# Performance work log

Measured on AMD Instinct MI355X. Metric: run time of the kernel, lower is better.

Reference implementation:

```python
import jax, jax.numpy as jnp
import numpy as np

NEG_W = 0.5  # negative_weight

def setup_inputs() -> dict:
    key = jax.random.key(0)
    ks = jax.random.split(key, 11)
    U, V, P, F, D, NF = 16384, 50000, 65536, 20, 64, 100000
    return {
        "user_emb": jax.random.normal(ks[0], (NF, D), jnp.float32),
        "item_emb": jax.random.normal(ks[1], (NF, D), jnp.float32),
        "w_user": jax.random.normal(ks[2], (NF,), jnp.float32),
        "w_item": jax.random.normal(ks[3], (NF,), jnp.float32),
        "bias": jax.random.normal(ks[4], (1,), jnp.float32),
        "h1": jax.random.normal(ks[5], (D,), jnp.float32),
        "h2": jax.random.normal(ks[6], (D,), jnp.float32),
        "user_feat_idx": jax.random.randint(ks[7], (U, F), 0, NF, jnp.int32),
        "item_feat_idx": jax.random.randint(ks[8], (V, F), 0, NF, jnp.int32),
        "pos_user_ids": jax.random.randint(ks[9], (P,), 0, U, jnp.int32),
        "pos_item_ids": jax.random.randint(ks[10], (P,), 0, V, jnp.int32),
    }

def _entity_terms(emb, w, feat_idx, h1, extra):
    # emb: [NF,D], feat_idx: [N,F] -> batched gather + FM bi-interaction
    g = emb[feat_idx]                      # [N,F,D]
    s = g.sum(axis=1)                      # [N,D]  (p_ud / q_vd)
    bi = 0.5 * (jnp.square(s) - jnp.square(g).sum(axis=1))  # [N,D]
    scalar = bi @ h1 + w[feat_idx].sum(axis=1) + extra       # [N]
    return s, scalar

def reference(user_emb, item_emb, w_user, w_item, bias, h1, h2,
              user_feat_idx, item_feat_idx, pos_user_ids, pos_item_ids):
    U = user_feat_idx.shape[0]
    V = item_feat_idx.shape[0]
    ones_u = jnp.ones((U, 1), user_emb.dtype)
    ones_v = jnp.ones((V, 1), item_emb.dtype)

    p_ud, su = _entity_terms(user_emb, w_user, user_feat_idx, h1, bias[0])
    q_vd, sv = _entity_terms(item_emb, w_item, item_feat_idx, h1, 0.0)
    p_u = jnp.concatenate([p_ud, su[:, None], ones_u], axis=1)  # [U,D+2]
    q_v = jnp.concatenate([q_vd, ones_v, sv[:, None]], axis=1)  # [V,D+2]

    # negative (all-pairs) term via D x D Gram matrices
    A = p_ud.T @ p_ud                                           # [D,D]
    B = q_vd.T @ q_vd                                           # [D,D]
    loss_neg = NEG_W * jnp.einsum('i,j,ij,ij->', h2, h2, A, B)

    # positive-pair term
    hv = jnp.concatenate([h2, jnp.ones((2,), h2.dtype)])        # [D+2]
    y = jnp.einsum('pd,pd,d->p', p_u[pos_user_ids], q_v[pos_item_ids], hv)
    loss_pos = jnp.sum((1.0 - NEG_W) * jnp.square(y) - 2.0 * y)

    return jnp.reshape(loss_neg + loss_pos, (1,))
```

## Files before the change

### kernel.cpp

```cpp
#include <hip/hip_runtime.h>

#define FD 20
#define DD 64

#define GA 64
#define GB 128
#define GAB 16
#define GBB 32
#define POSB 2048
#define NEGB 64

typedef float float4v __attribute__((ext_vector_type(4)));
typedef unsigned short ushort4v __attribute__((ext_vector_type(4)));
typedef unsigned short ushort8v __attribute__((ext_vector_type(8)));
typedef short short8v __attribute__((ext_vector_type(8)));

__device__ __forceinline__ unsigned short f2bf(float f) {
    unsigned u = __float_as_uint(f);
    unsigned r = u + 0x7fffu + ((u >> 16) & 1u);
    return (unsigned short)(r >> 16);
}
__device__ __forceinline__ float bf2f(unsigned short h) {
    return __uint_as_float((unsigned)h << 16);
}

__global__ __launch_bounds__(256) void conv_kernel(
    const float* __restrict__ ue, const float* __restrict__ ie,
    unsigned int* __restrict__ u8, unsigned int* __restrict__ i8,
    int n4, float* __restrict__ out, int out_size)
{
    int i = blockIdx.x * blockDim.x + threadIdx.x;
    if (i < out_size) out[i] = 0.0f;
    if (i >= 2 * n4) return;
    const float4v* src; unsigned int* dst; int k;
    if (i < n4) { src = (const float4v*)ue; dst = u8; k = i; }
    else        { src = (const float4v*)ie; dst = i8; k = i - n4; }
    float4v v = src[k];
    unsigned int p = 0;
    p = __builtin_amdgcn_cvt_pk_fp8_f32(v.x, v.y, p, false);
    p = __builtin_amdgcn_cvt_pk_fp8_f32(v.z, v.w, p, true);
    dst[k] = p;
}

__global__ __launch_bounds__(256, 4) void entity_kernel(
    const unsigned char* __restrict__ user_f8,
    const unsigned char* __restrict__ item_f8,
    const float* __restrict__ w_user, const float* __restrict__ w_item,
    const float* __restrict__ bias, const float* __restrict__ h1,
    const int* __restrict__ ufeat, const int* __restrict__ ifeat,
    unsigned short* __restrict__ p_bf, float* __restrict__ su,
    unsigned short* __restrict__ q_bf, float* __restrict__ sv,
    int U, int V)
{
    int wid  = (int)((blockIdx.x * blockDim.x + threadIdx.x) >> 6);
    int lane = threadIdx.x & 63;
    if (wid >= U + V) return;

    const unsigned char* emb; const float* wv; const int* fidx; float extra;
    unsigned short* srow; float* sc;
    if (wid < U) {
        emb = user_f8; wv = w_user; fidx = ufeat + (size_t)wid * FD;
        extra = bias[0]; srow = p_bf + (size_t)wid * DD; sc = su + wid;
    } else {
        int m = wid - U;
        emb = item_f8; wv = w_item; fidx = ifeat + (size_t)m * FD;
        extra = 0.0f; srow = q_bf + (size_t)m * DD; sc = sv + m;
    }

    int myidx = 0; float myw = 0.0f;
    if (lane < FD) {
        myidx = fidx[lane];
        myw   = wv[myidx];
    }

    int grp = lane >> 4;
    int c   = lane & 15;

    int fx[5];
#pragma unroll
    for (int i = 0; i < 5; ++i)
        fx[i] = __shfl(myidx, grp + 4 * i, 64);

    unsigned int hw[5];
#pragma unroll
    for (int i = 0; i < 5; ++i)
        hw[i] = *((const unsigned int*)(emb + (size_t)fx[i] * DD) + c);

    float4v s4 = (float4v)0.0f, ss4 = (float4v)0.0f;
#pragma unroll
    for (int i = 0; i < 5; ++i) {
        float4v g;
        g.x = __builtin_amdgcn_cvt_f32_fp8(hw[i], 0);
        g.y = __builtin_amdgcn_cvt_f32_fp8(hw[i], 1);
        g.z = __builtin_amdgcn_cvt_f32_fp8(hw[i], 2);
        g.w = __builtin_amdgcn_cvt_f32_fp8(hw[i], 3);
        s4 += g; ss4 += g * g;
    }

#pragma unroll
    for (int off = 16; off <= 32; off <<= 1) {
        float4v t, u;
        t.x = __shfl_xor(s4.x,  off, 64); t.y = __shfl_xor(s4.y,  off, 64);
        t.z = __shfl_xor(s4.z,  off, 64); t.w = __shfl_xor(s4.w,  off, 64);
        u.x = __shfl_xor(ss4.x, off, 64); u.y = __shfl_xor(ss4.y, off, 64);
        u.z = __shfl_xor(ss4.z, off, 64); u.w = __shfl_xor(ss4.w, off, 64);
        s4 += t; ss4 += u;
    }

    float part = myw;
    if (grp == 0) {
        float4v h14 = *(const float4v*)(h1 + c * 4);
        float4v bi4 = 0.5f * (s4 * s4 - ss4);
        part += bi4.x*h14.x + bi4.y*h14.y + bi4.z*h14.z + bi4.w*h14.w;
        ushort4v o;
        o.x = f2bf(s4.x); o.y = f2bf(s4.y); o.z = f2bf(s4.z); o.w = f2bf(s4.w);
        *(ushort4v*)(srow + c * 4) = o;
    }

#pragma unroll
    for (int off = 1; off <= 32; off <<= 1)
        part += __shfl_xor(part, off, 64);

    if (lane == 0) *sc = part + extra;
}

__device__ __forceinline__ void gram_block_mfma(
    const unsigned short* __restrict__ M, int nrows, int gwid, int nw,
    float* __restrict__ Gpart, unsigned short* __restrict__ sm)
{
    int lane = threadIdx.x & 63;
    int q = lane >> 4;
    int c = lane & 15;

    float4v acc[10];
#pragma unroll
    for (int t = 0; t < 10; ++t) acc[t] = (float4v)0.0f;

    int ntiles = (nrows + 63) >> 6;
    for (int tt = gwid; tt < ntiles; tt += nw) {
        int row0 = tt << 6;
#pragma unroll
        for (int p = 0; p < 8; ++p) {
            int r  = p * 8 + (lane >> 3);
            int ch = lane & 7;
            ushort8v hv = (ushort8v)0;
            if (row0 + r < nrows)
                hv = *(const ushort8v*)(M + (size_t)(row0 + r) * DD + ch * 8);
            int X = (p & 3) << 1;
            *(ushort8v*)(sm + r * 64 + ((ch ^ X) << 3)) = hv;
        }
#pragma unroll
        for (int kb2 = 0; kb2 < 2; ++kb2) {
            int k0 = kb2 * 32 + q * 8;
            int X  = q << 1;
            const unsigned short* rb = sm + k0 * 64 + (c & 7);
            short8v f[4];
#pragma unroll
            for (int Db = 0; Db < 4; ++Db) {
                int chunk = (Db * 2 + (c >> 3)) ^ X;
                const unsigned short* b = rb + chunk * 8;
                short8v fv;
#pragma unroll
                for (int j = 0; j < 8; ++j)
                    fv[j] = (short)b[j * 64];
                f[Db] = fv;
            }
#define MM(i_, j_, t_) acc[t_] = __builtin_amdgcn_mfma_f32_16x16x32_bf16(f[i_], f[j_], acc[t_], 0, 0, 0);
            MM(0,0,0) MM(0,1,1) MM(0,2,2) MM(0,3,3) MM(1,1,4)
            MM(1,2,5) MM(1,3,6) MM(2,2,7) MM(2,3,8) MM(3,3,9)
#undef MM
        }
    }

    float* out = Gpart + (size_t)gwid * (DD * DD);
#define ST(i_, j_, t_)                                                     \
    {                                                                      \
        for (int rg = 0; rg < 4; ++rg)                                     \
            out[(i_ * 16 + q * 4 + rg) * DD + j_ * 16 + c] = acc[t_][rg];  \
    }
    ST(0,0,0) ST(0,1,1) ST(0,2,2) ST(0,3,3) ST(1,1,4)
    ST(1,2,5) ST(1,3,6) ST(2,2,7) ST(2,3,8) ST(3,3,9)
#undef ST
}

__global__ __launch_bounds__(256) void mid_kernel(
    const unsigned short* __restrict__ p_bf, int U, float* __restrict__ PA,
    const unsigned short* __restrict__ q_bf, int V, float* __restrict__ PB,
    const float* __restrict__ su, const float* __restrict__ sv,
    const float* __restrict__ h2,
    const int* __restrict__ pu, const int* __restrict__ pi,
    int P, float* __restrict__ posPart)
{
    __shared__ unsigned short gtiles[4][64 * 64];
    __shared__ float red[4];
    int w = threadIdx.x >> 6;

    if (blockIdx.x < GAB) {
        gram_block_mfma(p_bf, U, blockIdx.x * 4 + w, GA, PA, gtiles[w]);
        return;
    }
    if (blockIdx.x < GAB + GBB) {
        gram_block_mfma(q_bf, V, (blockIdx.x - GAB) * 4 + w, GB, PB, gtiles[w]);
        return;
    }

    int lane = threadIdx.x & 63;
    int sl   = lane & 15;
    int sub  = lane >> 4;
    int pb   = blockIdx.x - (GAB + GBB);
    int wId  = pb * 4 + (threadIdx.x >> 6);
    const int NW = POSB * 4;

    float4v h2v = *(const float4v*)(h2 + sl * 4);

    int pid0 = wId * 4 + sub;
    int pid1 = pid0 + NW * 4;
    bool ok0 = pid0 < P, ok1 = pid1 < P;

    int u0 = 0, v0 = 0, u1 = 0, v1 = 0;
    if (ok0) { u0 = pu[pid0]; v0 = pi[pid0]; }
    if (ok1) { u1 = pu[pid1]; v1 = pi[pid1]; }

    ushort4v ph0 = (ushort4v)0, qh0 = (ushort4v)0;
    ushort4v ph1 = (ushort4v)0, qh1 = (ushort4v)0;
    if (ok0) {
        ph0 = *(const ushort4v*)(p_bf + (size_t)u0 * DD + sl * 4);
        qh0 = *(const ushort4v*)(q_bf + (size_t)v0 * DD + sl * 4);
    }
    if (ok1) {
        ph1 = *(const ushort4v*)(p_bf + (size_t)u1 * DD + sl * 4);
        qh1 = *(const ushort4v*)(q_bf + (size_t)v1 * DD + sl * 4);
    }

    float d0 = bf2f(ph0.x)*bf2f(qh0.x)*h2v.x + bf2f(ph0.y)*bf2f(qh0.y)*h2v.y
             + bf2f(ph0.z)*bf2f(qh0.z)*h2v.z + bf2f(ph0.w)*bf2f(qh0.w)*h2v.w;
    float d1 = bf2f(ph1.x)*bf2f(qh1.x)*h2v.x + bf2f(ph1.y)*bf2f(qh1.y)*h2v.y
             + bf2f(ph1.z)*bf2f(qh1.z)*h2v.z + bf2f(ph1.w)*bf2f(qh1.w)*h2v.w;
#pragma unroll
    for (int off = 1; off < 16; off <<= 1) {
        d0 += __shfl_xor(d0, off, 64);
        d1 += __shfl_xor(d1, off, 64);
    }

    float acc = 0.0f;
    if (sl == 0) {
        if (ok0) { float y = d0 + su[u0] + sv[v0]; acc += 0.5f * y * y - 2.0f * y; }
        if (ok1) { float y = d1 + su[u1] + sv[v1]; acc += 0.5f * y * y - 2.0f * y; }
    }
    acc += __shfl_xor(acc, 16, 64);
    acc += __shfl_xor(acc, 32, 64);
    if (lane == 0) red[threadIdx.x >> 6] = acc;
    __syncthreads();
    if (threadIdx.x == 0)
        posPart[pb] = red[0] + red[1] + red[2] + red[3];
}

__global__ __launch_bounds__(256) void neg_reduce_kernel(
    const float* __restrict__ PA, const float* __restrict__ PB,
    const float* __restrict__ h2, const float* __restrict__ posPart,
    float* __restrict__ out)
{
    __shared__ float sA[4][64], sB[4][64];
    __shared__ float sPos;
    int t  = threadIdx.x;
    int l  = t & 63;
    int ch = t >> 6;
    int i  = blockIdx.x;
    int e  = ((i >> 4) <= (l >> 4)) ? (i * 64 + l) : (l * 64 + i);

    float a = 0.0f, b = 0.0f;
#pragma unroll
    for (int k = 0; k < GA / 4; ++k)
        a += PA[(size_t)(ch * (GA / 4) + k) * (DD * DD) + e];
#pragma unroll
    for (int k = 0; k < GB / 4; ++k)
        b += PB[(size_t)(ch * (GB / 4) + k) * (DD * DD) + e];
    sA[ch][l] = a;
    sB[ch][l] = b;

    if (ch == 1) {
        float p = (l < POSB / NEGB) ? posPart[blockIdx.x * (POSB / NEGB) + l] : 0.0f;
#pragma unroll
        for (int off = 1; off <= 32; off <<= 1)
            p += __shfl_xor(p, off, 64);
        if (l == 0) sPos = p;
    }
    __syncthreads();

    if (ch == 0) {
        float fa = sA[0][l] + sA[1][l] + sA[2][l] + sA[3][l];
        float fb = sB[0][l] + sB[1][l] + sB[2][l] + sB[3][l];
        float acc = 0.5f * h2[blockIdx.x] * h2[l] * fa * fb;
#pragma unroll
        for (int off = 1; off <= 32; off <<= 1)
            acc += __shfl_xor(acc, off, 64);
        if (l == 0)
            atomicAdd(out, acc + sPos);
    }
}

extern "C" void kernel_launch(void* const* d_in, const int* in_sizes, int n_in,
                              void* d_out, int out_size, void* d_ws, size_t ws_size,
                              hipStream_t stream)
{
    const float* user_emb = (const float*)d_in[0];
    const float* item_emb = (const float*)d_in[1];
    const float* w_user   = (const float*)d_in[2];
    const float* w_item   = (const float*)d_in[3];
    const float* bias     = (const float*)d_in[4];
    const float* h1       = (const float*)d_in[5];
    const float* h2       = (const float*)d_in[6];
    const int*   ufeat    = (const int*)d_in[7];
    const int*   ifeat    = (const int*)d_in[8];
    const int*   pu       = (const int*)d_in[9];
    const int*   pi       = (const int*)d_in[10];

    const int NF = in_sizes[0] / DD;
    const int U  = in_sizes[7] / FD;
    const int V  = in_sizes[8] / FD;
    const int P  = in_sizes[9];

    float* ws = (float*)d_ws;
    size_t off = 0;
    unsigned short* p_bf = (unsigned short*)(ws + off); off += (size_t)U * DD / 2;
    unsigned short* q_bf = (unsigned short*)(ws + off); off += (size_t)V * DD / 2;
    float* su   = ws + off; off += (size_t)U;          off = (off + 63) & ~(size_t)63;
    float* sv   = ws + off; off += (size_t)V;          off = (off + 63) & ~(size_t)63;
    float* PA   = ws + off; off += (size_t)GA * DD * DD;
    float* PB   = ws + off; off += (size_t)GB * DD * DD;
    float* posPart = ws + off; off += (size_t)POSB;    off = (off + 63) & ~(size_t)63;
    unsigned char* uf8 = (unsigned char*)(ws + off);   off += (size_t)NF * DD / 4;
    unsigned char* if8 = (unsigned char*)(ws + off);   off += (size_t)NF * DD / 4;

    float* out = (float*)d_out;

    int n4 = NF * DD / 4;
    conv_kernel<<<(2 * n4 + 255) / 256, 256, 0, stream>>>(
        user_emb, item_emb, (unsigned int*)uf8, (unsigned int*)if8,
        n4, out, out_size);

    int nent = U + V;
    entity_kernel<<<(nent + 3) / 4, 256, 0, stream>>>(
        uf8, if8, w_user, w_item, bias, h1,
        ufeat, ifeat, p_bf, su, q_bf, sv, U, V);

    mid_kernel<<<GAB + GBB + POSB, 256, 0, stream>>>(
        p_bf, U, PA, q_bf, V, PB, su, sv, h2, pu, pi, P, posPart);

    neg_reduce_kernel<<<NEGB, 256, 0, stream>>>(PA, PB, h2, posPart, out);
}
```

Baseline: 168.0 us.

## Load Gram MFMA fragments directly from global and compute full 4x4 tile grid

The Gram-matrix routine no longer stages 64x64 bf16 tiles through LDS. Each lane now gathers its MFMA operand fragments straight from global memory with strided 2-byte loads, and the separate bounds-checked path is used only for the tail tile. It also computes all 16 16x16 output blocks instead of the 10 upper-triangle ones, so the reduction kernel can index entries directly without the symmetric mirroring. The aim is to drop LDS traffic, the LDS allocation and the store/load round trip, at the cost of 60% more MFMA work and uncoalesced scalar global loads.

Result: faster. 148.5 us (-11.6%).

```diff
diff --git a/kernel.cpp b/kernel.cpp
--- a/kernel.cpp
+++ b/kernel.cpp
@@ -126,61 +126,59 @@
 
 __device__ __forceinline__ void gram_block_mfma(
     const unsigned short* __restrict__ M, int nrows, int gwid, int nw,
-    float* __restrict__ Gpart, unsigned short* __restrict__ sm)
+    float* __restrict__ Gpart)
 {
     int lane = threadIdx.x & 63;
     int q = lane >> 4;
     int c = lane & 15;
 
-    float4v acc[10];
-#pragma unroll
-    for (int t = 0; t < 10; ++t) acc[t] = (float4v)0.0f;
+    float4v acc[4][4];
+#pragma unroll
+    for (int ti = 0; ti < 4; ++ti)
+#pragma unroll
+        for (int tj = 0; tj < 4; ++tj)
+            acc[ti][tj] = (float4v)0.0f;
 
     int ntiles = (nrows + 63) >> 6;
     for (int tt = gwid; tt < ntiles; tt += nw) {
         int row0 = tt << 6;
 #pragma unroll
-        for (int p = 0; p < 8; ++p) {
-            int r  = p * 8 + (lane >> 3);
-            int ch = lane & 7;
-            ushort8v hv = (ushort8v)0;
-            if (row0 + r < nrows)
-                hv = *(const ushort8v*)(M + (size_t)(row0 + r) * DD + ch * 8);
-            int X = (p & 3) << 1;
-            *(ushort8v*)(sm + r * 64 + ((ch ^ X) << 3)) = hv;
+        for (int kb = 0; kb < 2; ++kb) {
+            int r0 = row0 + kb * 32 + q * 8;
+            const unsigned short* base = M + (size_t)r0 * DD + c;
+            short8v f[4];
+            if (row0 + 64 <= nrows) {
+#pragma unroll
+                for (int Db = 0; Db < 4; ++Db)
+#pragma unroll
+                    for (int j = 0; j < 8; ++j)
+                        f[Db][j] = (short)base[(size_t)j * DD + Db * 16];
+            } else {
+#pragma unroll
+                for (int Db = 0; Db < 4; ++Db)
+#pragma unroll
+                    for (int j = 0; j < 8; ++j)
+                        f[Db][j] = (r0 + j < nrows)
+                                 ? (short)base[(size_t)j * DD + Db * 16]
+                                 : (short)0;
+            }
+#pragma unroll
+            for (int ti = 0; ti < 4; ++ti)
+#pragma unroll
+                for (int tj = 0; tj < 4; ++tj)
+                    acc[ti][tj] = __builtin_amdgcn_mfma_f32_16x16x32_bf16(
+                        f[ti], f[tj], acc[ti][tj], 0, 0, 0);
         }
-#pragma unroll
-        for (int kb2 = 0; kb2 < 2; ++kb2) {
-            int k0 = kb2 * 32 + q * 8;
-            int X  = q << 1;
-            const unsigned short* rb = sm + k0 * 64 + (c & 7);
-            short8v f[4];
-#pragma unroll
-            for (int Db = 0; Db < 4; ++Db) {
-                int chunk = (Db * 2 + (c >> 3)) ^ X;
-                const unsigned short* b = rb + chunk * 8;
-                short8v fv;
-#pragma unroll
-                for (int j = 0; j < 8; ++j)
-                    fv[j] = (short)b[j * 64];
-                f[Db] = fv;
-            }
-#define MM(i_, j_, t_) acc[t_] = __builtin_amdgcn_mfma_f32_16x16x32_bf16(f[i_], f[j_], acc[t_], 0, 0, 0);
-            MM(0,0,0) MM(0,1,1) MM(0,2,2) MM(0,3,3) MM(1,1,4)
-            MM(1,2,5) MM(1,3,6) MM(2,2,7) MM(2,3,8) MM(3,3,9)
-#undef MM
-        }
     }
 
     float* out = Gpart + (size_t)gwid * (DD * DD);
-#define ST(i_, j_, t_)                                                     \
-    {                                                                      \
-        for (int rg = 0; rg < 4; ++rg)                                     \
-            out[(i_ * 16 + q * 4 + rg) * DD + j_ * 16 + c] = acc[t_][rg];  \
-    }
-    ST(0,0,0) ST(0,1,1) ST(0,2,2) ST(0,3,3) ST(1,1,4)
-    ST(1,2,5) ST(1,3,6) ST(2,2,7) ST(2,3,8) ST(3,3,9)
-#undef ST
+#pragma unroll
+    for (int ti = 0; ti < 4; ++ti)
+#pragma unroll
+        for (int tj = 0; tj < 4; ++tj)
+#pragma unroll
+            for (int rg = 0; rg < 4; ++rg)
+                out[(ti * 16 + q * 4 + rg) * DD + tj * 16 + c] = acc[ti][tj][rg];
 }
 
 __global__ __launch_bounds__(256) void mid_kernel(
@@ -191,16 +189,15 @@
     const int* __restrict__ pu, const int* __restrict__ pi,
     int P, float* __restrict__ posPart)
 {
-    __shared__ unsigned short gtiles[4][64 * 64];
     __shared__ float red[4];
     int w = threadIdx.x >> 6;
 
     if (blockIdx.x < GAB) {
-        gram_block_mfma(p_bf, U, blockIdx.x * 4 + w, GA, PA, gtiles[w]);
+        gram_block_mfma(p_bf, U, blockIdx.x * 4 + w, GA, PA);
         return;
     }
     if (blockIdx.x < GAB + GBB) {
-        gram_block_mfma(q_bf, V, (blockIdx.x - GAB) * 4 + w, GB, PB, gtiles[w]);
+        gram_block_mfma(q_bf, V, (blockIdx.x - GAB) * 4 + w, GB, PB);
         return;
     }
 
@@ -208,7 +205,7 @@
     int sl   = lane & 15;
     int sub  = lane >> 4;
     int pb   = blockIdx.x - (GAB + GBB);
-    int wId  = pb * 4 + (threadIdx.x >> 6);
+    int wId  = pb * 4 + w;
     const int NW = POSB * 4;
 
     float4v h2v = *(const float4v*)(h2 + sl * 4);
@@ -249,7 +246,7 @@
     }
     acc += __shfl_xor(acc, 16, 64);
     acc += __shfl_xor(acc, 32, 64);
-    if (lane == 0) red[threadIdx.x >> 6] = acc;
+    if (lane == 0) red[w] = acc;
     __syncthreads();
     if (threadIdx.x == 0)
         posPart[pb] = red[0] + red[1] + red[2] + red[3];
@@ -265,8 +262,7 @@
     int t  = threadIdx.x;
     int l  = t & 63;
     int ch = t >> 6;
-    int i  = blockIdx.x;
-    int e  = ((i >> 4) <= (l >> 4)) ? (i * 64 + l) : (l * 64 + i);
+    int e  = blockIdx.x * 64 + l;
 
     float a = 0.0f, b = 0.0f;
 #pragma unroll
```
